# Kernel optimization log

Hardware: AMD Instinct MI355X
Metric: run time of the kernel (lower is better)

Reference implementation:

```python
import jax, jax.numpy as jnp
import numpy as np

N_A, N_G, D, H = 100000, 25000, 128, 4
E_B, E_O, E_R, E_P = 400000, 100000, 200000, 200000
BN_INV = float(1.0 / np.sqrt(1.0 + 1e-5))  # eval-mode BatchNorm1d, running mean 0 / var 1


def setup_inputs():
    key = jax.random.key(0)
    ks = iter(jax.random.split(key, 64))
    nrm = lambda shape, s=0.05: jax.random.normal(next(ks), shape, jnp.float32) * s
    ri = lambda n, hi: jax.random.randint(next(ks), (n,), 0, hi, jnp.int32)
    inp = dict(
        x_atom=nrm((N_A, D), 1.0), x_group=nrm((N_G, D), 1.0),
        ef_bond=nrm((E_B, D), 1.0), ef_overlap=nrm((E_O, D), 1.0),
        bond_src=ri(E_B, N_A), bond_dst=ri(E_B, N_A),
        ov_src=ri(E_O, N_G), ov_dst=ri(E_O, N_G),
        ref_src=ri(E_R, N_G), ref_dst=ri(E_R, N_A),
        pool_src=ri(E_P, N_A), pool_dst=ri(E_P, N_G),
    )
    # two GINE convs (bond 'b', overlap 'o'): eps + MLP Linear(D,2D)->BN->ReLU->Linear(2D,D)
    for pre in ('b', 'o'):
        inp[pre + '_eps'] = jnp.zeros((1,), jnp.float32)
        inp[pre + '_W1'] = nrm((D, 2 * D)); inp[pre + '_b1'] = jnp.zeros((2 * D,), jnp.float32)
        inp[pre + '_g1'] = jnp.ones((2 * D,), jnp.float32); inp[pre + '_be1'] = jnp.zeros((2 * D,), jnp.float32)
        inp[pre + '_W2'] = nrm((2 * D, D)); inp[pre + '_b2'] = jnp.zeros((D,), jnp.float32)
    # two ModifiedGATConvs (refine 'r', pool 'p'): GATConv + Flatten->BN->ReLU->Linear
    for pre in ('r', 'p'):
        inp[pre + '_Wfc'] = nrm((D, H * D)); inp[pre + '_al'] = nrm((H, D)); inp[pre + '_ar'] = nrm((H, D))
        inp[pre + '_Wres'] = nrm((D, H * D)); inp[pre + '_bias'] = jnp.zeros((H * D,), jnp.float32)
        inp[pre + '_g'] = jnp.ones((H * D,), jnp.float32); inp[pre + '_b'] = jnp.zeros((H * D,), jnp.float32)
        inp[pre + '_Wout'] = nrm((H * D, D)); inp[pre + '_bout'] = jnp.zeros((D,), jnp.float32)
    return inp


def _gine(x_src, x_dst, efeat, src, dst, n_dst, eps, W1, b1, g1, be1, W2, b2):
    m = jax.nn.relu(x_src[src] + efeat)                       # [E, D] message: relu(h_src + e)
    neigh = jax.ops.segment_sum(m, dst, num_segments=n_dst)   # [Nd, D] sum-reduce
    h = (1.0 + eps) * x_dst + neigh
    h = h @ W1 + b1
    h = jax.nn.relu(g1 * (h * BN_INV) + be1)                  # eval BN
    return h @ W2 + b2


def _gat(x_src, x_dst, src, dst, n_dst, Wfc, al, ar, Wres, bias, g, b, Wout, bout):
    hs = (x_src @ Wfc).reshape(-1, H, D)                      # [Ns, H, D]
    hd = (x_dst @ Wfc).reshape(-1, H, D)
    el = jnp.sum(hs * al, axis=-1)                            # [Ns, H]
    er = jnp.sum(hd * ar, axis=-1)                            # [Nd, H]
    e = jax.nn.leaky_relu(el[src] + er[dst], 0.2)             # [E, H]
    emax = jax.ops.segment_max(e, dst, num_segments=n_dst)    # per-dst softmax (stable)
    ex = jnp.exp(e - emax[dst])
    den = jax.ops.segment_sum(ex, dst, num_segments=n_dst)
    a = ex / jnp.maximum(den[dst], 1e-9)                      # [E, H]
    rst = jax.ops.segment_sum(a[:, :, None] * hs[src], dst, num_segments=n_dst)  # [Nd, H, D]
    rst = rst + (x_dst @ Wres).reshape(-1, H, D) + bias.reshape(H, D)            # residual + bias
    flat = rst.reshape(-1, H * D)                             # Flatten
    h = jax.nn.relu(g * (flat * BN_INV) + b)                  # eval BN -> ReLU
    return h @ Wout + bout


def reference(x_atom, x_group, ef_bond, ef_overlap, bond_src, bond_dst, ov_src, ov_dst, ref_src, ref_dst, pool_src, pool_dst, b_eps, b_W1, b_b1, b_g1, b_be1, b_W2, b_b2, o_eps, o_W1, o_b1, o_g1, o_be1, o_W2, o_b2, r_Wfc, r_al, r_ar, r_Wres, r_bias, r_g, r_b, r_Wout, r_bout, p_Wfc, p_al, p_ar, p_Wres, p_bias, p_g, p_b, p_Wout, p_bout):
    # HeteroGraphConv with default 'sum' cross-relation aggregation per dst node type
    out_atom = _gine(x_atom, x_atom, ef_bond, bond_src, bond_dst, N_A, b_eps, b_W1, b_b1, b_g1, b_be1, b_W2, b_b2)
    out_atom = out_atom + _gat(x_group, x_atom, ref_src, ref_dst, N_A, r_Wfc, r_al, r_ar, r_Wres, r_bias, r_g, r_b, r_Wout, r_bout)
    out_group = _gine(x_group, x_group, ef_overlap, ov_src, ov_dst, N_G, o_eps, o_W1, o_b1, o_g1, o_be1, o_W2, o_b2)
    out_group = out_group + _gat(x_atom, x_group, pool_src, pool_dst, N_G, p_Wfc, p_al, p_ar, p_Wres, p_bias, p_g, p_b, p_Wout, p_bout)
    return jnp.concatenate([out_atom, out_group], axis=0)     # [N_A + N_G, D]
```

## Files before the change

kernel.cpp:

```cpp
#include <hip/hip_runtime.h>
#include <hip/hip_bf16.h>

#define N_A 100000
#define N_G 25000
#define DD 128
#define E_B 400000
#define E_O 100000
#define E_R 200000
#define E_P 200000
#define CAP 256

static constexpr float BN_INV_C = 0.99999500003749969f;

typedef __attribute__((ext_vector_type(8))) short bf16x8;
typedef __attribute__((ext_vector_type(4))) float f32x4;

__device__ __forceinline__ unsigned short f2bf(float f) {
    unsigned u = __float_as_uint(f);
    unsigned r = (u + 0x7FFFu + ((u >> 16) & 1u)) >> 16;
    return (unsigned short)r;
}
__device__ __forceinline__ float bf2f(unsigned short s) {
    return __uint_as_float(((unsigned)s) << 16);
}
__device__ __forceinline__ float lrelu(float v) { return v > 0.f ? v : 0.2f * v; }

__global__ void k_xcast_all(const float* __restrict__ xa, const float* __restrict__ xg,
                            unsigned short* __restrict__ xab, unsigned short* __restrict__ xgb) {
    int t = blockIdx.x * blockDim.x + threadIdx.x;
    if (t < N_A * 32) {
        float4 v = *(const float4*)(xa + (size_t)t * 4);
        ushort4 o; o.x = f2bf(v.x); o.y = f2bf(v.y); o.z = f2bf(v.z); o.w = f2bf(v.w);
        *(ushort4*)(xab + (size_t)t * 4) = o;
    } else {
        int t2 = t - N_A * 32;
        if (t2 >= N_G * 32) return;
        float4 v = *(const float4*)(xg + (size_t)t2 * 4);
        ushort4 o; o.x = f2bf(v.x); o.y = f2bf(v.y); o.z = f2bf(v.z); o.w = f2bf(v.w);
        *(ushort4*)(xgb + (size_t)t2 * 4) = o;
    }
}

struct WcSeg { const float* src; unsigned short* dst; int K; int N; int ldk; int off; };
struct WcArgs { WcSeg s[10]; };

__global__ void k_wcast_all(WcArgs a) {
    WcSeg sg = a.s[blockIdx.y];
    int t = blockIdx.x * blockDim.x + threadIdx.x;
    if (t >= sg.K * sg.N) return;
    int n = t % sg.N, k = t / sg.N;
    sg.dst[(size_t)n * sg.ldk + sg.off + k] = f2bf(sg.src[t]);
}

__global__ void k_war_all(const float* __restrict__ rWfc, const float* __restrict__ ral,
                          const float* __restrict__ rar, const float* __restrict__ pWfc,
                          const float* __restrict__ pal, const float* __restrict__ par,
                          float* __restrict__ wv) {
    int bsel = blockIdx.x;
    const float* W = bsel < 2 ? rWfc : pWfc;
    const float* vec = bsel == 0 ? ral : bsel == 1 ? rar : bsel == 2 ? pal : par;
    float* o = wv + bsel * 512;
    int t = threadIdx.x;
    int k = t >> 2, h = t & 3;
    const float* wr = W + (size_t)k * 512 + h * 128;
    const float* av = vec + h * 128;
    float s = 0.f;
    for (int d = 0; d < 128; ++d) s += wr[d] * av[d];
    o[t] = s;
}

__global__ void k_ll_build_all(const int* __restrict__ bd, const int* __restrict__ od,
                               const int* __restrict__ rd, const int* __restrict__ pd,
                               int* __restrict__ heads, int* __restrict__ nxt) {
    int t = blockIdx.x * blockDim.x + threadIdx.x;
    if (t < E_B) {
        nxt[t] = atomicExch(&heads[bd[t]], t);
    } else if (t < E_B + E_O) {
        int e = t - E_B;
        nxt[E_B + e] = atomicExch(&heads[100000 + od[e]], e);
    } else if (t < E_B + E_O + E_R) {
        int e = t - E_B - E_O;
        nxt[E_B + E_O + e] = atomicExch(&heads[125000 + rd[e]], e);
    } else if (t < E_B + E_O + E_R + E_P) {
        int e = t - E_B - E_O - E_R;
        nxt[E_B + E_O + E_R + e] = atomicExch(&heads[225000 + pd[e]], e);
    }
}

__global__ __launch_bounds__(64) void k_gine_gather_all(
    const unsigned short* __restrict__ xAb, const unsigned short* __restrict__ xGb,
    const float* __restrict__ efB, const float* __restrict__ efO,
    const int* __restrict__ bsrc, const int* __restrict__ osrc,
    const int* __restrict__ heads, const int* __restrict__ nxt,
    const float* __restrict__ beps, const float* __restrict__ oeps,
    unsigned short* __restrict__ h0A, unsigned short* __restrict__ h0G) {
    int n = blockIdx.x, lane = threadIdx.x;
    const unsigned short* xs; const unsigned short* xdrow; const float* ef;
    const int* esrc; const int* hd; const int* nx; float ep; unsigned short* outp; int nn;
    if (n < N_A) {
        nn = n; xs = xAb; xdrow = xAb + (size_t)n * DD; ef = efB; esrc = bsrc;
        hd = heads; nx = nxt; ep = 1.0f + beps[0]; outp = h0A + (size_t)n * DD;
    } else {
        nn = n - N_A; xs = xGb; xdrow = xGb + (size_t)nn * DD; ef = efO; esrc = osrc;
        hd = heads + 100000; nx = nxt + E_B; ep = 1.0f + oeps[0]; outp = h0G + (size_t)nn * DD;
    }
    float2 acc = make_float2(0.f, 0.f);
    for (int e = hd[nn]; e >= 0; e = nx[e]) {
        int s = esrc[e];
        unsigned xa = *(const unsigned*)(xs + (size_t)s * DD + lane * 2);
        float2 ev = *(const float2*)(ef + (size_t)e * DD + lane * 2);
        acc.x += fmaxf(bf2f((unsigned short)(xa & 0xffff)) + ev.x, 0.f);
        acc.y += fmaxf(bf2f((unsigned short)(xa >> 16)) + ev.y, 0.f);
    }
    unsigned xd = *(const unsigned*)(xdrow + lane * 2);
    float rx = ep * bf2f((unsigned short)(xd & 0xffff)) + acc.x;
    float ry = ep * bf2f((unsigned short)(xd >> 16)) + acc.y;
    *(unsigned*)(outp + lane * 2) = (unsigned)f2bf(rx) | ((unsigned)f2bf(ry) << 16);
}

__global__ void k_el_all(const unsigned short* __restrict__ xAb,
                         const unsigned short* __restrict__ xGb,
                         const float* __restrict__ wv,
                         float* __restrict__ elR, float* __restrict__ elP) {
    int t = blockIdx.x * blockDim.x + threadIdx.x;
    const unsigned short* xr; const float* wvp; float* op; int idx;
    if (t < N_G * 4) {
        idx = t; xr = xGb + (size_t)(t >> 2) * DD; wvp = wv; op = elR;
    } else {
        int t2 = t - N_G * 4;
        if (t2 >= N_A * 4) return;
        idx = t2; xr = xAb + (size_t)(t2 >> 2) * DD; wvp = wv + 1024; op = elP;
    }
    int h = idx & 3;
    float s = 0.f;
#pragma unroll
    for (int k = 0; k < DD; k += 8) {
        uint4 w = *(const uint4*)(xr + k);
        unsigned wa[4] = {w.x, w.y, w.z, w.w};
#pragma unroll
        for (int q = 0; q < 4; ++q) {
            s += bf2f((unsigned short)(wa[q] & 0xffff)) * wvp[(k + q * 2) * 4 + h];
            s += bf2f((unsigned short)(wa[q] >> 16)) * wvp[(k + q * 2 + 1) * 4 + h];
        }
    }
    op[idx] = s;
}

__global__ __launch_bounds__(64) void k_att_gather_all(
    const unsigned short* __restrict__ xAb, const unsigned short* __restrict__ xGb,
    const float* __restrict__ elR, const float* __restrict__ elP,
    const float* __restrict__ wv,
    const int* __restrict__ rsrc, const int* __restrict__ psrc,
    const int* __restrict__ heads, const int* __restrict__ nxt,
    unsigned short* __restrict__ A2r, unsigned short* __restrict__ A2p) {
    int n = blockIdx.x, lane = threadIdx.x;
    const unsigned short* xs; const unsigned short* xdrow; const float* el;
    const float* wvr; const int* esrc; const int* hd; const int* nx;
    unsigned short* A2; int nn;
    if (n < N_A) {
        nn = n; xs = xGb; xdrow = xAb + (size_t)n * DD; el = elR; wvr = wv + 512;
        esrc = rsrc; hd = heads + 125000; nx = nxt + (E_B + E_O);
        A2 = A2r + (size_t)n * 512;
    } else {
        nn = n - N_A; xs = xAb; xdrow = xGb + (size_t)nn * DD; el = elP; wvr = wv + 1536;
        esrc = psrc; hd = heads + 225000; nx = nxt + (E_B + E_O + E_R);
        A2 = A2p + (size_t)nn * 512;
    }
    __shared__ int slist[CAP];
    __shared__ float sa[4][CAP];
    unsigned xd = *(const unsigned*)(xdrow + lane * 2);
    float xd0 = bf2f((unsigned short)(xd & 0xffff));
    float xd1 = bf2f((unsigned short)(xd >> 16));
    float er[4];
#pragma unroll
    for (int h = 0; h < 4; ++h)
        er[h] = xd0 * wvr[(2 * lane) * 4 + h] + xd1 * wvr[(2 * lane + 1) * 4 + h];
#pragma unroll
    for (int m = 1; m < 64; m <<= 1) {
#pragma unroll
        for (int h = 0; h < 4; ++h) er[h] += __shfl_xor(er[h], m, 64);
    }
    int cnt = 0, erest = -1;
    for (int e = hd[nn]; e >= 0; e = nx[e]) {
        if (cnt < CAP) {
            if (lane == 0) slist[cnt] = esrc[e];
            cnt++;
        } else {
            erest = e;
            break;
        }
    }
    __syncthreads();
    float mx[4] = {-1e30f, -1e30f, -1e30f, -1e30f};
    for (int i = lane; i < cnt; i += 64) {
        int s = slist[i];
        float4 e4 = *(const float4*)(el + (size_t)s * 4);
        float l0 = lrelu(e4.x + er[0]);
        float l1 = lrelu(e4.y + er[1]);
        float l2 = lrelu(e4.z + er[2]);
        float l3 = lrelu(e4.w + er[3]);
        sa[0][i] = l0; sa[1][i] = l1; sa[2][i] = l2; sa[3][i] = l3;
        mx[0] = fmaxf(mx[0], l0); mx[1] = fmaxf(mx[1], l1);
        mx[2] = fmaxf(mx[2], l2); mx[3] = fmaxf(mx[3], l3);
    }
#pragma unroll
    for (int m = 1; m < 64; m <<= 1) {
#pragma unroll
        for (int h = 0; h < 4; ++h) mx[h] = fmaxf(mx[h], __shfl_xor(mx[h], m, 64));
    }
    for (int e = erest; e >= 0; e = nx[e]) {
        int s = esrc[e];
        float4 e4 = *(const float4*)(el + (size_t)s * 4);
        mx[0] = fmaxf(mx[0], lrelu(e4.x + er[0]));
        mx[1] = fmaxf(mx[1], lrelu(e4.y + er[1]));
        mx[2] = fmaxf(mx[2], lrelu(e4.z + er[2]));
        mx[3] = fmaxf(mx[3], lrelu(e4.w + er[3]));
    }
    float den[4] = {0.f, 0.f, 0.f, 0.f};
    for (int i = lane; i < cnt; i += 64) {
        float v0 = __expf(sa[0][i] - mx[0]);
        float v1 = __expf(sa[1][i] - mx[1]);
        float v2 = __expf(sa[2][i] - mx[2]);
        float v3 = __expf(sa[3][i] - mx[3]);
        sa[0][i] = v0; sa[1][i] = v1; sa[2][i] = v2; sa[3][i] = v3;
        den[0] += v0; den[1] += v1; den[2] += v2; den[3] += v3;
    }
#pragma unroll
    for (int m = 1; m < 64; m <<= 1) {
#pragma unroll
        for (int h = 0; h < 4; ++h) den[h] += __shfl_xor(den[h], m, 64);
    }
    for (int e = erest; e >= 0; e = nx[e]) {
        int s = esrc[e];
        float4 e4 = *(const float4*)(el + (size_t)s * 4);
        den[0] += __expf(lrelu(e4.x + er[0]) - mx[0]);
        den[1] += __expf(lrelu(e4.y + er[1]) - mx[1]);
        den[2] += __expf(lrelu(e4.z + er[2]) - mx[2]);
        den[3] += __expf(lrelu(e4.w + er[3]) - mx[3]);
    }
    float inv[4];
#pragma unroll
    for (int h = 0; h < 4; ++h) inv[h] = 1.f / fmaxf(den[h], 1e-9f);
    __syncthreads();
    float acc[4][2] = {};
    for (int i = 0; i < cnt; ++i) {
        int s = slist[i];
        float a0 = sa[0][i] * inv[0];
        float a1 = sa[1][i] * inv[1];
        float a2 = sa[2][i] * inv[2];
        float a3 = sa[3][i] * inv[3];
        unsigned xw = *(const unsigned*)(xs + (size_t)s * DD + lane * 2);
        float x0 = bf2f((unsigned short)(xw & 0xffff));
        float x1 = bf2f((unsigned short)(xw >> 16));
        acc[0][0] += a0 * x0; acc[0][1] += a0 * x1;
        acc[1][0] += a1 * x0; acc[1][1] += a1 * x1;
        acc[2][0] += a2 * x0; acc[2][1] += a2 * x1;
        acc[3][0] += a3 * x0; acc[3][1] += a3 * x1;
    }
    for (int e = erest; e >= 0; e = nx[e]) {
        int s = esrc[e];
        float4 e4 = *(const float4*)(el + (size_t)s * 4);
        unsigned xw = *(const unsigned*)(xs + (size_t)s * DD + lane * 2);
        float x0 = bf2f((unsigned short)(xw & 0xffff));
        float x1 = bf2f((unsigned short)(xw >> 16));
        float a0 = __expf(lrelu(e4.x + er[0]) - mx[0]) * inv[0];
        float a1 = __expf(lrelu(e4.y + er[1]) - mx[1]) * inv[1];
        float a2 = __expf(lrelu(e4.z + er[2]) - mx[2]) * inv[2];
        float a3 = __expf(lrelu(e4.w + er[3]) - mx[3]) * inv[3];
        acc[0][0] += a0 * x0; acc[0][1] += a0 * x1;
        acc[1][0] += a1 * x0; acc[1][1] += a1 * x1;
        acc[2][0] += a2 * x0; acc[2][1] += a2 * x1;
        acc[3][0] += a3 * x0; acc[3][1] += a3 * x1;
    }
#pragma unroll
    for (int h = 0; h < 4; ++h) {
        unsigned o = (unsigned)f2bf(acc[h][0]) | ((unsigned)f2bf(acc[h][1]) << 16);
        *(unsigned*)(A2 + h * 128 + lane * 2) = o;
    }
}

#define LDKP 40
template <int EPI, int OUTBF, int GATK>
__global__ __launch_bounds__(256) void k_gemm_bf(
    const unsigned short* __restrict__ A, const unsigned short* __restrict__ Bt,
    void* __restrict__ C, int M, int N, int K,
    const float* __restrict__ bias, const float* __restrict__ g,
    const float* __restrict__ be, const unsigned short* __restrict__ addbf,
    const unsigned short* __restrict__ Axd) {
    __shared__ unsigned short As[128 * LDKP];
    __shared__ unsigned short Bs[128 * LDKP];
    int tid = threadIdx.x;
    int wave = tid >> 6, lane = tid & 63;
    int wr = wave >> 1, wc = wave & 1;
    int row0 = blockIdx.y * 128, col0 = blockIdx.x * 128;
    int l16 = lane & 15, khalf = (lane >> 4) * 8;
    f32x4 acc[4][4] = {};
    int r_0 = tid >> 2, ko_0 = (tid & 3) * 8;
    int r_1 = (tid + 256) >> 2, ko_1 = ((tid + 256) & 3) * 8;
    for (int k0 = 0; k0 < K; k0 += 32) {
        __syncthreads();
        {
            int kk = k0 + ko_0;
            int ra = min(row0 + r_0, M - 1);
            uint4 va;
            if (GATK) va = (kk < 128) ? *(const uint4*)(A + (size_t)ra * 512 + col0 + kk)
                                      : *(const uint4*)(Axd + (size_t)ra * 128 + (kk - 128));
            else va = *(const uint4*)(A + (size_t)ra * K + kk);
            *(uint4*)(&As[r_0 * LDKP + ko_0]) = va;
            uint4 vb = *(const uint4*)(Bt + (size_t)(col0 + r_0) * K + kk);
            *(uint4*)(&Bs[r_0 * LDKP + ko_0]) = vb;
            kk = k0 + ko_1;
            ra = min(row0 + r_1, M - 1);
            if (GATK) va = (kk < 128) ? *(const uint4*)(A + (size_t)ra * 512 + col0 + kk)
                                      : *(const uint4*)(Axd + (size_t)ra * 128 + (kk - 128));
            else va = *(const uint4*)(A + (size_t)ra * K + kk);
            *(uint4*)(&As[r_1 * LDKP + ko_1]) = va;
            vb = *(const uint4*)(Bt + (size_t)(col0 + r_1) * K + kk);
            *(uint4*)(&Bs[r_1 * LDKP + ko_1]) = vb;
        }
        __syncthreads();
        bf16x8 af[4], bfr[4];
#pragma unroll
        for (int i = 0; i < 4; ++i)
            af[i] = *(const bf16x8*)(&As[(wr * 64 + i * 16 + l16) * LDKP + khalf]);
#pragma unroll
        for (int j = 0; j < 4; ++j)
            bfr[j] = *(const bf16x8*)(&Bs[(wc * 64 + j * 16 + l16) * LDKP + khalf]);
#pragma unroll
        for (int i = 0; i < 4; ++i)
#pragma unroll
            for (int j = 0; j < 4; ++j)
                acc[i][j] = __builtin_amdgcn_mfma_f32_16x16x32_bf16(af[i], bfr[j], acc[i][j], 0, 0, 0);
    }
    int rq = (lane >> 4) * 4;
#pragma unroll
    for (int i = 0; i < 4; ++i) {
#pragma unroll
        for (int reg = 0; reg < 4; ++reg) {
            int r = row0 + wr * 64 + i * 16 + rq + reg;
            if (r >= M) continue;
#pragma unroll
            for (int j = 0; j < 4; ++j) {
                int c = col0 + wc * 64 + j * 16 + l16;
                float v = acc[i][j][reg];
                size_t idx = (size_t)r * N + c;
                v += bias[c];
                if (EPI == 2) {
                    v = g[c] * (v * BN_INV_C) + be[c];
                    v = fmaxf(v, 0.f);
                }
                if (EPI == 3) {
                    ((float*)C)[idx] = v + bf2f(addbf[idx]);
                } else if (OUTBF) {
                    ((unsigned short*)C)[idx] = f2bf(v);
                } else {
                    ((float*)C)[idx] = v;
                }
            }
        }
    }
}

extern "C" void kernel_launch(void* const* d_in, const int* in_sizes, int n_in,
                              void* d_out, int out_size, void* d_ws, size_t ws_size,
                              hipStream_t stream) {
    const float* x_atom = (const float*)d_in[0];
    const float* x_group = (const float*)d_in[1];
    const float* ef_bond = (const float*)d_in[2];
    const float* ef_ov = (const float*)d_in[3];
    const int* bond_src = (const int*)d_in[4];
    const int* bond_dst = (const int*)d_in[5];
    const int* ov_src = (const int*)d_in[6];
    const int* ov_dst = (const int*)d_in[7];
    const int* ref_src = (const int*)d_in[8];
    const int* ref_dst = (const int*)d_in[9];
    const int* pool_src = (const int*)d_in[10];
    const int* pool_dst = (const int*)d_in[11];
    const float* b_eps = (const float*)d_in[12];
    const float* b_W1 = (const float*)d_in[13];
    const float* b_b1 = (const float*)d_in[14];
    const float* b_g1 = (const float*)d_in[15];
    const float* b_be1 = (const float*)d_in[16];
    const float* b_W2 = (const float*)d_in[17];
    const float* b_b2 = (const float*)d_in[18];
    const float* o_eps = (const float*)d_in[19];
    const float* o_W1 = (const float*)d_in[20];
    const float* o_b1 = (const float*)d_in[21];
    const float* o_g1 = (const float*)d_in[22];
    const float* o_be1 = (const float*)d_in[23];
    const float* o_W2 = (const float*)d_in[24];
    const float* o_b2 = (const float*)d_in[25];
    const float* r_Wfc = (const float*)d_in[26];
    const float* r_al = (const float*)d_in[27];
    const float* r_ar = (const float*)d_in[28];
    const float* r_Wres = (const float*)d_in[29];
    const float* r_bias = (const float*)d_in[30];
    const float* r_g = (const float*)d_in[31];
    const float* r_b = (const float*)d_in[32];
    const float* r_Wout = (const float*)d_in[33];
    const float* r_bout = (const float*)d_in[34];
    const float* p_Wfc = (const float*)d_in[35];
    const float* p_al = (const float*)d_in[36];
    const float* p_ar = (const float*)d_in[37];
    const float* p_Wres = (const float*)d_in[38];
    const float* p_bias = (const float*)d_in[39];
    const float* p_g = (const float*)d_in[40];
    const float* p_b = (const float*)d_in[41];
    const float* p_Wout = (const float*)d_in[42];
    const float* p_bout = (const float*)d_in[43];

    float* out = (float*)d_out;
    char* wsb = (char*)d_ws;
    unsigned short* xAb = (unsigned short*)(wsb + 0);
    unsigned short* xGb = (unsigned short*)(wsb + 26000000);
    unsigned short* WtB1 = (unsigned short*)(wsb + 33000000);
    unsigned short* WtB2 = WtB1 + 32768;
    unsigned short* WtO1 = WtB2 + 32768;
    unsigned short* WtO2 = WtO1 + 32768;
    unsigned short* WtR  = WtO2 + 32768;
    unsigned short* WtRo = WtR + 131072;
    unsigned short* WtP  = WtRo + 65536;
    unsigned short* WtPo = WtP + 131072;
    float* wv   = (float*)(wsb + 34100000);
    float* elR  = (float*)(wsb + 34200000);
    float* elP  = (float*)(wsb + 34600000);
    int* heads  = (int*)(wsb + 36300000);
    int* nxt    = (int*)(wsb + 37400000);
    unsigned short* h0A = (unsigned short*)(wsb + 41100000);
    unsigned short* h0G = (unsigned short*)(wsb + 66800000);
    unsigned short* R4  = (unsigned short*)(wsb + 73300000);
    unsigned short* G1a = (unsigned short*)(wsb + 124600000);
    unsigned short* G1g = (unsigned short*)(wsb + 150300000);
    unsigned short* A2r = (unsigned short*)(wsb + 156800000);
    unsigned short* A2p = (unsigned short*)(wsb + 259300000);
    unsigned short* R3r = (unsigned short*)(wsb + 285000000);
    unsigned short* R3p = (unsigned short*)(wsb + 387500000);

    k_xcast_all<<<((N_A + N_G) * 32 + 255) / 256, 256, 0, stream>>>(x_atom, x_group, xAb, xGb);
    WcArgs wa;
    wa.s[0] = {b_W1, WtB1, 128, 256, 128, 0};
    wa.s[1] = {b_W2, WtB2, 256, 128, 256, 0};
    wa.s[2] = {o_W1, WtO1, 128, 256, 128, 0};
    wa.s[3] = {o_W2, WtO2, 256, 128, 256, 0};
    wa.s[4] = {r_Wfc, WtR, 128, 512, 256, 0};
    wa.s[5] = {r_Wres, WtR, 128, 512, 256, 128};
    wa.s[6] = {r_Wout, WtRo, 512, 128, 512, 0};
    wa.s[7] = {p_Wfc, WtP, 128, 512, 256, 0};
    wa.s[8] = {p_Wres, WtP, 128, 512, 256, 128};
    wa.s[9] = {p_Wout, WtPo, 512, 128, 512, 0};
    k_wcast_all<<<dim3(256, 10), 256, 0, stream>>>(wa);
    k_war_all<<<4, 512, 0, stream>>>(r_Wfc, r_al, r_ar, p_Wfc, p_al, p_ar, wv);
    hipMemsetAsync(heads, 0xFF, 250000 * 4, stream);
    k_ll_build_all<<<(E_B + E_O + E_R + E_P + 255) / 256, 256, 0, stream>>>(
        bond_dst, ov_dst, ref_dst, pool_dst, heads, nxt);
    k_gine_gather_all<<<N_A + N_G, 64, 0, stream>>>(xAb, xGb, ef_bond, ef_ov, bond_src, ov_src,
                                                    heads, nxt, b_eps, o_eps, h0A, h0G);
    k_gemm_bf<2, 1, 0><<<dim3(2, 782), 256, 0, stream>>>(h0A, WtB1, R4, N_A, 256, 128, b_b1, b_g1, b_be1, nullptr, nullptr);
    k_gemm_bf<1, 1, 0><<<dim3(1, 782), 256, 0, stream>>>(R4, WtB2, G1a, N_A, 128, 256, b_b2, nullptr, nullptr, nullptr, nullptr);
    k_gemm_bf<2, 1, 0><<<dim3(2, 196), 256, 0, stream>>>(h0G, WtO1, R4, N_G, 256, 128, o_b1, o_g1, o_be1, nullptr, nullptr);
    k_gemm_bf<1, 1, 0><<<dim3(1, 196), 256, 0, stream>>>(R4, WtO2, G1g, N_G, 128, 256, o_b2, nullptr, nullptr, nullptr, nullptr);
    k_el_all<<<((N_G + N_A) * 4 + 255) / 256, 256, 0, stream>>>(xAb, xGb, wv, elR, elP);
    k_att_gather_all<<<N_A + N_G, 64, 0, stream>>>(xAb, xGb, elR, elP, wv, ref_src, pool_src,
                                                   heads, nxt, A2r, A2p);
    k_gemm_bf<2, 1, 1><<<dim3(4, 782), 256, 0, stream>>>(A2r, WtR, R3r, N_A, 512, 256, r_bias, r_g, r_b, nullptr, xAb);
    k_gemm_bf<2, 1, 1><<<dim3(4, 196), 256, 0, stream>>>(A2p, WtP, R3p, N_G, 512, 256, p_bias, p_g, p_b, nullptr, xGb);
    k_gemm_bf<3, 0, 0><<<dim3(1, 782), 256, 0, stream>>>(R3r, WtRo, out, N_A, 128, 512, r_bout, nullptr, nullptr, G1a, nullptr);
    k_gemm_bf<3, 0, 0><<<dim3(1, 196), 256, 0, stream>>>(R3p, WtPo, out + (size_t)N_A * DD, N_G, 128, 512, p_bout, nullptr, nullptr, G1g, nullptr);
}
```

Baseline: 609.3 us.

## Replace linked-list adjacency with fixed-stride bucketed adjacency plus overflow list

Builds a per-destination fixed-stride (64) adjacency array of (edge, src) pairs using atomicAdd degree counters, falling back to the old linked list only for overflow edges. The gather kernels then read neighbor lists with one coalesced load into shared memory instead of chasing dependent next pointers, which removes serialized pointer-chasing latency. Gather kernels also pack four nodes per 256-thread block for better occupancy. The cost is a large extra workspace buffer, an extra memset, and scattered 8-byte writes during construction.

```diff
diff --git a/kernel.cpp b/kernel.cpp
--- a/kernel.cpp
+++ b/kernel.cpp
@@ -8,7 +8,9 @@
 #define E_O 100000
 #define E_R 200000
 #define E_P 200000
-#define CAP 256
+#define EALL 900000
+#define NSLOT 250000
+#define STRIDE 64
 
 static constexpr float BN_INV_C = 0.99999500003749969f;
 
@@ -69,48 +71,67 @@
     o[t] = s;
 }
 
-__global__ void k_ll_build_all(const int* __restrict__ bd, const int* __restrict__ od,
-                               const int* __restrict__ rd, const int* __restrict__ pd,
-                               int* __restrict__ heads, int* __restrict__ nxt) {
+__global__ void k_adj_fill(const int* __restrict__ bs, const int* __restrict__ bd,
+                           const int* __restrict__ os, const int* __restrict__ od,
+                           const int* __restrict__ rs, const int* __restrict__ rd,
+                           const int* __restrict__ ps, const int* __restrict__ pd,
+                           int* __restrict__ deg, uint2* __restrict__ adj,
+                           int* __restrict__ heads, int* __restrict__ nxt) {
     int t = blockIdx.x * blockDim.x + threadIdx.x;
-    if (t < E_B) {
-        nxt[t] = atomicExch(&heads[bd[t]], t);
-    } else if (t < E_B + E_O) {
-        int e = t - E_B;
-        nxt[E_B + e] = atomicExch(&heads[100000 + od[e]], e);
-    } else if (t < E_B + E_O + E_R) {
-        int e = t - E_B - E_O;
-        nxt[E_B + E_O + e] = atomicExch(&heads[125000 + rd[e]], e);
-    } else if (t < E_B + E_O + E_R + E_P) {
-        int e = t - E_B - E_O - E_R;
-        nxt[E_B + E_O + E_R + e] = atomicExch(&heads[225000 + pd[e]], e);
-    }
-}
-
-__global__ __launch_bounds__(64) void k_gine_gather_all(
+    int e, base, go; const int* S; const int* D;
+    if (t < E_B) { e = t; S = bs; D = bd; base = 0; go = 0; }
+    else if (t < E_B + E_O) { e = t - E_B; S = os; D = od; base = 100000; go = E_B; }
+    else if (t < E_B + E_O + E_R) { e = t - (E_B + E_O); S = rs; D = rd; base = 125000; go = E_B + E_O; }
+    else if (t < EALL) { e = t - (E_B + E_O + E_R); S = ps; D = pd; base = 225000; go = E_B + E_O + E_R; }
+    else return;
+    int d = D[e], s = S[e];
+    int ns = base + d;
+    int pos = atomicAdd(&deg[ns], 1);
+    if (pos < STRIDE) adj[(size_t)ns * STRIDE + pos] = make_uint2((unsigned)e, (unsigned)s);
+    else nxt[go + e] = atomicExch(&heads[ns], e);
+}
+
+__global__ __launch_bounds__(256) void k_gine_gather_all(
     const unsigned short* __restrict__ xAb, const unsigned short* __restrict__ xGb,
     const float* __restrict__ efB, const float* __restrict__ efO,
     const int* __restrict__ bsrc, const int* __restrict__ osrc,
+    const int* __restrict__ deg, const uint2* __restrict__ adj,
     const int* __restrict__ heads, const int* __restrict__ nxt,
     const float* __restrict__ beps, const float* __restrict__ oeps,
     unsigned short* __restrict__ h0A, unsigned short* __restrict__ h0G) {
-    int n = blockIdx.x, lane = threadIdx.x;
+    int wid = threadIdx.x >> 6, lane = threadIdx.x & 63;
+    int n = blockIdx.x * 4 + wid;
+    __shared__ uint2 gl[4][STRIDE];
     const unsigned short* xs; const unsigned short* xdrow; const float* ef;
-    const int* esrc; const int* hd; const int* nx; float ep; unsigned short* outp; int nn;
+    const int* esrc; const int* nx; float ep; unsigned short* outp; int nn, base, go;
     if (n < N_A) {
         nn = n; xs = xAb; xdrow = xAb + (size_t)n * DD; ef = efB; esrc = bsrc;
-        hd = heads; nx = nxt; ep = 1.0f + beps[0]; outp = h0A + (size_t)n * DD;
+        base = 0; go = 0; ep = 1.0f + beps[0]; outp = h0A + (size_t)n * DD;
     } else {
         nn = n - N_A; xs = xGb; xdrow = xGb + (size_t)nn * DD; ef = efO; esrc = osrc;
-        hd = heads + 100000; nx = nxt + E_B; ep = 1.0f + oeps[0]; outp = h0G + (size_t)nn * DD;
-    }
+        base = 100000; go = E_B; ep = 1.0f + oeps[0]; outp = h0G + (size_t)nn * DD;
+    }
+    nx = nxt + go;
+    int d = deg[base + nn];
+    int cb = min(d, STRIDE);
+    if (lane < cb) gl[wid][lane] = adj[(size_t)(base + nn) * STRIDE + lane];
+    __syncthreads();
     float2 acc = make_float2(0.f, 0.f);
-    for (int e = hd[nn]; e >= 0; e = nx[e]) {
-        int s = esrc[e];
-        unsigned xa = *(const unsigned*)(xs + (size_t)s * DD + lane * 2);
-        float2 ev = *(const float2*)(ef + (size_t)e * DD + lane * 2);
+    for (int i = 0; i < cb; ++i) {
+        uint2 es = gl[wid][i];
+        unsigned xa = *(const unsigned*)(xs + (size_t)es.y * DD + lane * 2);
+        float2 ev = *(const float2*)(ef + (size_t)es.x * DD + lane * 2);
         acc.x += fmaxf(bf2f((unsigned short)(xa & 0xffff)) + ev.x, 0.f);
         acc.y += fmaxf(bf2f((unsigned short)(xa >> 16)) + ev.y, 0.f);
+    }
+    if (d > STRIDE) {
+        for (int e = heads[base + nn]; e >= 0; e = nx[e]) {
+            int s = esrc[e];
+            unsigned xa = *(const unsigned*)(xs + (size_t)s * DD + lane * 2);
+            float2 ev = *(const float2*)(ef + (size_t)e * DD + lane * 2);
+            acc.x += fmaxf(bf2f((unsigned short)(xa & 0xffff)) + ev.x, 0.f);
+            acc.y += fmaxf(bf2f((unsigned short)(xa >> 16)) + ev.y, 0.f);
+        }
     }
     unsigned xd = *(const unsigned*)(xdrow + lane * 2);
     float rx = ep * bf2f((unsigned short)(xd & 0xffff)) + acc.x;
@@ -146,28 +167,35 @@
     op[idx] = s;
 }
 
-__global__ __launch_bounds__(64) void k_att_gather_all(
+__global__ __launch_bounds__(256) void k_att_gather_all(
     const unsigned short* __restrict__ xAb, const unsigned short* __restrict__ xGb,
     const float* __restrict__ elR, const float* __restrict__ elP,
     const float* __restrict__ wv,
     const int* __restrict__ rsrc, const int* __restrict__ psrc,
+    const int* __restrict__ deg, const uint2* __restrict__ adj,
     const int* __restrict__ heads, const int* __restrict__ nxt,
     unsigned short* __restrict__ A2r, unsigned short* __restrict__ A2p) {
-    int n = blockIdx.x, lane = threadIdx.x;
+    int wid = threadIdx.x >> 6, lane = threadIdx.x & 63;
+    int n = blockIdx.x * 4 + wid;
+    __shared__ int sl[4][STRIDE];
+    __shared__ float sa[4][4][STRIDE];
     const unsigned short* xs; const unsigned short* xdrow; const float* el;
-    const float* wvr; const int* esrc; const int* hd; const int* nx;
-    unsigned short* A2; int nn;
+    const float* wvr; const int* esrc; const int* nx;
+    unsigned short* A2; int nn, base, go;
     if (n < N_A) {
         nn = n; xs = xGb; xdrow = xAb + (size_t)n * DD; el = elR; wvr = wv + 512;
-        esrc = rsrc; hd = heads + 125000; nx = nxt + (E_B + E_O);
+        esrc = rsrc; base = 125000; go = E_B + E_O;
         A2 = A2r + (size_t)n * 512;
     } else {
         nn = n - N_A; xs = xAb; xdrow = xGb + (size_t)nn * DD; el = elP; wvr = wv + 1536;
-        esrc = psrc; hd = heads + 225000; nx = nxt + (E_B + E_O + E_R);
+        esrc = psrc; base = 225000; go = E_B + E_O + E_R;
         A2 = A2p + (size_t)nn * 512;
     }
-    __shared__ int slist[CAP];
-    __shared__ float sa[4][CAP];
+    nx = nxt + go;
+    int d = deg[base + nn];
+    int cb = min(d, STRIDE);
+    if (lane < cb) sl[wid][lane] = (int)adj[(size_t)(base + nn) * STRIDE + lane].y;
+    __syncthreads();
     unsigned xd = *(const unsigned*)(xdrow + lane * 2);
     float xd0 = bf2f((unsigned short)(xd & 0xffff));
     float xd1 = bf2f((unsigned short)(xd >> 16));
@@ -180,75 +208,66 @@
 #pragma unroll
         for (int h = 0; h < 4; ++h) er[h] += __shfl_xor(er[h], m, 64);
     }
-    int cnt = 0, erest = -1;
-    for (int e = hd[nn]; e >= 0; e = nx[e]) {
-        if (cnt < CAP) {
-            if (lane == 0) slist[cnt] = esrc[e];
-            cnt++;
-        } else {
-            erest = e;
-            break;
-        }
-    }
-    __syncthreads();
     float mx[4] = {-1e30f, -1e30f, -1e30f, -1e30f};
-    for (int i = lane; i < cnt; i += 64) {
-        int s = slist[i];
+    float lv[4] = {0.f, 0.f, 0.f, 0.f};
+    if (lane < cb) {
+        int s = sl[wid][lane];
         float4 e4 = *(const float4*)(el + (size_t)s * 4);
-        float l0 = lrelu(e4.x + er[0]);
-        float l1 = lrelu(e4.y + er[1]);
-        float l2 = lrelu(e4.z + er[2]);
-        float l3 = lrelu(e4.w + er[3]);
-        sa[0][i] = l0; sa[1][i] = l1; sa[2][i] = l2; sa[3][i] = l3;
-        mx[0] = fmaxf(mx[0], l0); mx[1] = fmaxf(mx[1], l1);
-        mx[2] = fmaxf(mx[2], l2); mx[3] = fmaxf(mx[3], l3);
+        lv[0] = lrelu(e4.x + er[0]); lv[1] = lrelu(e4.y + er[1]);
+        lv[2] = lrelu(e4.z + er[2]); lv[3] = lrelu(e4.w + er[3]);
+#pragma unroll
+        for (int h = 0; h < 4; ++h) mx[h] = lv[h];
     }
 #pragma unroll
     for (int m = 1; m < 64; m <<= 1) {
 #pragma unroll
         for (int h = 0; h < 4; ++h) mx[h] = fmaxf(mx[h], __shfl_xor(mx[h], m, 64));
     }
-    for (int e = erest; e >= 0; e = nx[e]) {
-        int s = esrc[e];
-        float4 e4 = *(const float4*)(el + (size_t)s * 4);
-        mx[0] = fmaxf(mx[0], lrelu(e4.x + er[0]));
-        mx[1] = fmaxf(mx[1], lrelu(e4.y + er[1]));
-        mx[2] = fmaxf(mx[2], lrelu(e4.z + er[2]));
-        mx[3] = fmaxf(mx[3], lrelu(e4.w + er[3]));
+    if (d > STRIDE) {
+        for (int e = heads[base + nn]; e >= 0; e = nx[e]) {
+            int s = esrc[e];
+            float4 e4 = *(const float4*)(el + (size_t)s * 4);
+            mx[0] = fmaxf(mx[0], lrelu(e4.x + er[0]));
+            mx[1] = fmaxf(mx[1], lrelu(e4.y + er[1]));
+            mx[2] = fmaxf(mx[2], lrelu(e4.z + er[2]));
+            mx[3] = fmaxf(mx[3], lrelu(e4.w + er[3]));
+        }
     }
     float den[4] = {0.f, 0.f, 0.f, 0.f};
-    for (int i = lane; i < cnt; i += 64) {
-        float v0 = __expf(sa[0][i] - mx[0]);
-        float v1 = __expf(sa[1][i] - mx[1]);
-        float v2 = __expf(sa[2][i] - mx[2]);
-        float v3 = __expf(sa[3][i] - mx[3]);
-        sa[0][i] = v0; sa[1][i] = v1; sa[2][i] = v2; sa[3][i] = v3;
-        den[0] += v0; den[1] += v1; den[2] += v2; den[3] += v3;
+    if (lane < cb) {
+#pragma unroll
+        for (int h = 0; h < 4; ++h) {
+            float v = __expf(lv[h] - mx[h]);
+            sa[wid][h][lane] = v;
+            den[h] = v;
+        }
     }
 #pragma unroll
     for (int m = 1; m < 64; m <<= 1) {
 #pragma unroll
         for (int h = 0; h < 4; ++h) den[h] += __shfl_xor(den[h], m, 64);
     }
-    for (int e = erest; e >= 0; e = nx[e]) {
-        int s = esrc[e];
-        float4 e4 = *(const float4*)(el + (size_t)s * 4);
-        den[0] += __expf(lrelu(e4.x + er[0]) - mx[0]);
-        den[1] += __expf(lrelu(e4.y + er[1]) - mx[1]);
-        den[2] += __expf(lrelu(e4.z + er[2]) - mx[2]);
-        den[3] += __expf(lrelu(e4.w + er[3]) - mx[3]);
+    if (d > STRIDE) {
+        for (int e = heads[base + nn]; e >= 0; e = nx[e]) {
+            int s = esrc[e];
+            float4 e4 = *(const float4*)(el + (size_t)s * 4);
+            den[0] += __expf(lrelu(e4.x + er[0]) - mx[0]);
+            den[1] += __expf(lrelu(e4.y + er[1]) - mx[1]);
+            den[2] += __expf(lrelu(e4.z + er[2]) - mx[2]);
+            den[3] += __expf(lrelu(e4.w + er[3]) - mx[3]);
+        }
     }
     float inv[4];
 #pragma unroll
     for (int h = 0; h < 4; ++h) inv[h] = 1.f / fmaxf(den[h], 1e-9f);
     __syncthreads();
     float acc[4][2] = {};
-    for (int i = 0; i < cnt; ++i) {
-        int s = slist[i];
-        float a0 = sa[0][i] * inv[0];
-        float a1 = sa[1][i] * inv[1];
-        float a2 = sa[2][i] * inv[2];
-        float a3 = sa[3][i] * inv[3];
+    for (int i = 0; i < cb; ++i) {
+        int s = sl[wid][i];
+        float a0 = sa[wid][0][i] * inv[0];
+        float a1 = sa[wid][1][i] * inv[1];
+        float a2 = sa[wid][2][i] * inv[2];
+        float a3 = sa[wid][3][i] * inv[3];
         unsigned xw = *(const unsigned*)(xs + (size_t)s * DD + lane * 2);
         float x0 = bf2f((unsigned short)(xw & 0xffff));
         float x1 = bf2f((unsigned short)(xw >> 16));
@@ -257,20 +276,22 @@
         acc[2][0] += a2 * x0; acc[2][1] += a2 * x1;
         acc[3][0] += a3 * x0; acc[3][1] += a3 * x1;
     }
-    for (int e = erest; e >= 0; e = nx[e]) {
-        int s = esrc[e];
-        float4 e4 = *(const float4*)(el + (size_t)s * 4);
-        unsigned xw = *(const unsigned*)(xs + (size_t)s * DD + lane * 2);
-        float x0 = bf2f((unsigned short)(xw & 0xffff));
-        float x1 = bf2f((unsigned short)(xw >> 16));
-        float a0 = __expf(lrelu(e4.x + er[0]) - mx[0]) * inv[0];
-        float a1 = __expf(lrelu(e4.y + er[1]) - mx[1]) * inv[1];
-        float a2 = __expf(lrelu(e4.z + er[2]) - mx[2]) * inv[2];
-        float a3 = __expf(lrelu(e4.w + er[3]) - mx[3]) * inv[3];
-        acc[0][0] += a0 * x0; acc[0][1] += a0 * x1;
-        acc[1][0] += a1 * x0; acc[1][1] += a1 * x1;
-        acc[2][0] += a2 * x0; acc[2][1] += a2 * x1;
-        acc[3][0] += a3 * x0; acc[3][1] += a3 * x1;
+    if (d > STRIDE) {
+        for (int e = heads[base + nn]; e >= 0; e = nx[e]) {
+            int s = esrc[e];
+            float4 e4 = *(const float4*)(el + (size_t)s * 4);
+            unsigned xw = *(const unsigned*)(xs + (size_t)s * DD + lane * 2);
+            float x0 = bf2f((unsigned short)(xw & 0xffff));
+            float x1 = bf2f((unsigned short)(xw >> 16));
+            float a0 = __expf(lrelu(e4.x + er[0]) - mx[0]) * inv[0];
+            float a1 = __expf(lrelu(e4.y + er[1]) - mx[1]) * inv[1];
+            float a2 = __expf(lrelu(e4.z + er[2]) - mx[2]) * inv[2];
+            float a3 = __expf(lrelu(e4.w + er[3]) - mx[3]) * inv[3];
+            acc[0][0] += a0 * x0; acc[0][1] += a0 * x1;
+            acc[1][0] += a1 * x0; acc[1][1] += a1 * x1;
+            acc[2][0] += a2 * x0; acc[2][1] += a2 * x1;
+            acc[3][0] += a3 * x0; acc[3][1] += a3 * x1;
+        }
     }
 #pragma unroll
     for (int h = 0; h < 4; ++h) {
@@ -435,6 +456,8 @@
     unsigned short* A2p = (unsigned short*)(wsb + 259300000);
     unsigned short* R3r = (unsigned short*)(wsb + 285000000);
     unsigned short* R3p = (unsigned short*)(wsb + 387500000);
+    uint2* adj  = (uint2*)(wsb + 414000000);
+    int* deg    = (int*)(wsb + 543000000);
 
     k_xcast_all<<<((N_A + N_G) * 32 + 255) / 256, 256, 0, stream>>>(x_atom, x_group, xAb, xGb);
     WcArgs wa;
@@ -450,18 +473,20 @@
     wa.s[9] = {p_Wout, WtPo, 512, 128, 512, 0};
     k_wcast_all<<<dim3(256, 10), 256, 0, stream>>>(wa);
     k_war_all<<<4, 512, 0, stream>>>(r_Wfc, r_al, r_ar, p_Wfc, p_al, p_ar, wv);
-    hipMemsetAsync(heads, 0xFF, 250000 * 4, stream);
-    k_ll_build_all<<<(E_B + E_O + E_R + E_P + 255) / 256, 256, 0, stream>>>(
-        bond_dst, ov_dst, ref_dst, pool_dst, heads, nxt);
-    k_gine_gather_all<<<N_A + N_G, 64, 0, stream>>>(xAb, xGb, ef_bond, ef_ov, bond_src, ov_src,
-                                                    heads, nxt, b_eps, o_eps, h0A, h0G);
+    hipMemsetAsync(deg, 0, NSLOT * 4, stream);
+    hipMemsetAsync(heads, 0xFF, NSLOT * 4, stream);
+    k_adj_fill<<<(EALL + 255) / 256, 256, 0, stream>>>(
+        bond_src, bond_dst, ov_src, ov_dst, ref_src, ref_dst, pool_src, pool_dst,
+        deg, adj, heads, nxt);
+    k_gine_gather_all<<<31250, 256, 0, stream>>>(xAb, xGb, ef_bond, ef_ov, bond_src, ov_src,
+                                                 deg, adj, heads, nxt, b_eps, o_eps, h0A, h0G);
     k_gemm_bf<2, 1, 0><<<dim3(2, 782), 256, 0, stream>>>(h0A, WtB1, R4, N_A, 256, 128, b_b1, b_g1, b_be1, nullptr, nullptr);
     k_gemm_bf<1, 1, 0><<<dim3(1, 782), 256, 0, stream>>>(R4, WtB2, G1a, N_A, 128, 256, b_b2, nullptr, nullptr, nullptr, nullptr);
     k_gemm_bf<2, 1, 0><<<dim3(2, 196), 256, 0, stream>>>(h0G, WtO1, R4, N_G, 256, 128, o_b1, o_g1, o_be1, nullptr, nullptr);
     k_gemm_bf<1, 1, 0><<<dim3(1, 196), 256, 0, stream>>>(R4, WtO2, G1g, N_G, 128, 256, o_b2, nullptr, nullptr, nullptr, nullptr);
     k_el_all<<<((N_G + N_A) * 4 + 255) / 256, 256, 0, stream>>>(xAb, xGb, wv, elR, elP);
-    k_att_gather_all<<<N_A + N_G, 64, 0, stream>>>(xAb, xGb, elR, elP, wv, ref_src, pool_src,
-                                                   heads, nxt, A2r, A2p);
+    k_att_gather_all<<<31250, 256, 0, stream>>>(xAb, xGb, elR, elP, wv, ref_src, pool_src,
+                                                deg, adj, heads, nxt, A2r, A2p);
     k_gemm_bf<2, 1, 1><<<dim3(4, 782), 256, 0, stream>>>(A2r, WtR, R3r, N_A, 512, 256, r_bias, r_g, r_b, nullptr, xAb);
     k_gemm_bf<2, 1, 1><<<dim3(4, 196), 256, 0, stream>>>(A2p, WtP, R3p, N_G, 512, 256, p_bias, p_g, p_b, nullptr, xGb);
     k_gemm_bf<3, 0, 0><<<dim3(1, 782), 256, 0, stream>>>(R3r, WtRo, out, N_A, 128, 512, r_bout, nullptr, nullptr, G1a, nullptr);
```

Result: no change. 607.1 us (-0.4%).
